# Performance work log

Measured on AMD Instinct MI355X. Metric: run time of the kernel, lower is better.

Reference implementation:

```python
import jax, jax.numpy as jnp
import numpy as np


def setup_inputs() -> dict:
    key = jax.random.key(0)
    x = jax.random.normal(key, (32, 512, 56, 56), dtype=jnp.float32)
    return {"x": x}


def reference(x):
    n, c, h, w = x.shape
    f = x.reshape(n, c, h * w)                       # (n, c, hw)
    f_norm = jax.nn.softmax(f * 7.0, axis=2)         # softmax over spatial
    bilinear = jnp.einsum('ncs,nds->ncd', f_norm, f) # (n, c, c)
    bilinear = jax.nn.softmax(bilinear, axis=2)      # softmax over channel 'keys'
    trilinear = jnp.einsum('ncd,nds->ncs', bilinear, f).reshape(n, c, h, w)
    trilinear = jax.lax.stop_gradient(trilinear)     # matches torch .detach()
    structure_att = jnp.sum(trilinear, axis=1, keepdims=True)  # (n, 1, h, w)
    return structure_att
```

## Files before the change

kernel.cpp:

```cpp
#include <hip/hip_runtime.h>
#include <stdint.h>


#define NB 32
#define CC 512
#define SS 3136
#define SCALE 7.0f
#define K7F 10.098865286222744f
#define INVK7F 0.09902102579427789f

typedef float f32x4 __attribute__((ext_vector_type(4)));
typedef _Float16 f16x8 __attribute__((ext_vector_type(8)));
typedef _Float16 f16x4 __attribute__((ext_vector_type(4)));
typedef _Float16 f16x2 __attribute__((ext_vector_type(2)));

__device__ inline unsigned short f2bf(float f) {
  unsigned int u = __float_as_uint(f);
  u += 0x7fffu + ((u >> 16) & 1u);
  return (unsigned short)(u >> 16);
}
__device__ inline float bf2f(unsigned short u) {
  return __uint_as_float((uint32_t)u << 16);
}

__device__ inline float fast_exp2(float v) {
  float r;
  asm("v_exp_f32 %0, %1" : "=v"(r) : "v"(v));
  return r;
}
__device__ inline uint32_t pk2h(float a, float b) {
  uint32_t r;
  asm("v_cvt_pkrtz_f16_f32 %0, %1, %2" : "=v"(r) : "v"(a), "v"(b));
  return r;
}
__device__ inline f16x8 exp2_f16x8(f16x8 h) {
  f16x8 r;
#pragma unroll
  for (int q = 0; q < 4; q++) {
    const float e0 = fast_exp2((float)h[2 * q]);
    const float e1 = fast_exp2((float)h[2 * q + 1]);
    ((uint32_t*)&r)[q] = pk2h(e0, e1);
  }
  return r;
}

__device__ inline float wredmax(float v) {
#pragma unroll
  for (int m = 32; m >= 1; m >>= 1) v = fmaxf(v, __shfl_xor(v, m, 64));
  return v;
}
__device__ inline float wredsum(float v) {
#pragma unroll
  for (int m = 32; m >= 1; m >>= 1) v += __shfl_xor(v, m, 64);
  return v;
}

__device__ inline void load_lds16(const void* g, void* l) {
  __builtin_amdgcn_global_load_lds(
      (const __attribute__((address_space(1))) void*)(uintptr_t)g,
      (__attribute__((address_space(3))) void*)(uintptr_t)l, 16, 0, 0);
}

__global__ __launch_bounds__(256) void k_prep(const float* __restrict__ x,
                                              unsigned short* __restrict__ t,
                                              float* __restrict__ inv7,
                                              float* __restrict__ mxv,
                                              float* __restrict__ esum) {
  const int row = blockIdx.x;
  const int tid = threadIdx.x;
  if (tid == 0) esum[row] = 0.f;
  const float4* xr = (const float4*)(x + (size_t)row * SS);
  float4 v0 = xr[tid];
  float4 v1 = xr[tid + 256];
  float4 v2 = xr[tid + 512];
  float4 v3 = (tid < 16) ? xr[768 + tid] : make_float4(-1e30f, -1e30f, -1e30f, -1e30f);

  float mx = fmaxf(fmaxf(fmaxf(v0.x, v0.y), fmaxf(v0.z, v0.w)),
             fmaxf(fmaxf(fmaxf(v1.x, v1.y), fmaxf(v1.z, v1.w)),
             fmaxf(fmaxf(fmaxf(v2.x, v2.y), fmaxf(v2.z, v2.w)),
                   fmaxf(fmaxf(v3.x, v3.y), fmaxf(v3.z, v3.w)))));
  __shared__ float redm[4], reds[4];
  mx = wredmax(mx);
  if ((tid & 63) == 0) redm[tid >> 6] = mx;
  __syncthreads();
  mx = fmaxf(fmaxf(redm[0], redm[1]), fmaxf(redm[2], redm[3]));

  float s = 0.f;
  f16x4 p0, p1, p2, p3;
#define TQ2(dst, i0, a0, a1)                                  \
  {                                                           \
    _Float16 h0 = (_Float16)(K7F * ((a0) - mx));              \
    _Float16 h1 = (_Float16)(K7F * ((a1) - mx));              \
    dst[i0] = h0; dst[i0 + 1] = h1;                           \
    uint32_t u = pk2h(fast_exp2((float)h0), fast_exp2((float)h1)); \
    f16x2 e2; *(uint32_t*)&e2 = u;                            \
    s += (float)e2[0] + (float)e2[1];                         \
  }
  TQ2(p0, 0, v0.x, v0.y) TQ2(p0, 2, v0.z, v0.w)
  TQ2(p1, 0, v1.x, v1.y) TQ2(p1, 2, v1.z, v1.w)
  TQ2(p2, 0, v2.x, v2.y) TQ2(p2, 2, v2.z, v2.w)
  TQ2(p3, 0, v3.x, v3.y) TQ2(p3, 2, v3.z, v3.w)
#undef TQ2
  s = wredsum(s);
  if ((tid & 63) == 0) reds[tid >> 6] = s;
  __syncthreads();

  f16x4* tr = (f16x4*)(t + (size_t)row * SS);
  tr[tid] = p0;
  tr[tid + 256] = p1;
  tr[tid + 512] = p2;
  if (tid < 16) tr[768 + tid] = p3;
  if (tid == 0) {
    const float stot = reds[0] + reds[1] + reds[2] + reds[3];
    inv7[row] = 1.0f / (K7F * stot);
    mxv[row] = mx;
  }
}

#define BM 128
#define BK 64
#define NT (SS / BK)

__global__ __launch_bounds__(256, 2) void k_gemm(const unsigned short* __restrict__ T,
                                                 unsigned short* __restrict__ P,
                                                 const float* __restrict__ inv7,
                                                 const float* __restrict__ mxv,
                                                 float* __restrict__ esum) {
  __shared__ unsigned short sA[2][BM * BK];
  __shared__ unsigned short sB[2][BM * BK];
  const int lin  = blockIdx.y * gridDim.x + blockIdx.x;
  const int xcd  = lin & 7;
  const int slot = lin >> 3;
  const int pair = xcd * 16 + (slot >> 2);
  const int n    = pair >> 2;
  const int tm   = (pair & 3) * BM;
  const int tn   = (slot & 3) * BM;
  const unsigned short* Ap = T + (size_t)n * CC * SS + (size_t)tm * SS;
  const unsigned short* Bp = T + (size_t)n * CC * SS + (size_t)tn * SS;
  const int tid  = threadIdx.x;
  const int lane = tid & 63;
  const int wave = tid >> 6;
  const int wm   = (wave >> 1) * 64;
  const int wn   = (wave & 1) * 64;
  const int quad = lane >> 4;
  const int rr   = lane & 15;

  int jb[4];
  const unsigned short *Aaddr[4], *Baddr[4];
#pragma unroll
  for (int tt = 0; tt < 4; tt++) {
    const int j  = ((tt << 2) + wave) * 64 + lane;
    const int r  = j >> 3;
    const int cg = (j & 7) ^ (r & 7);
    jb[tt]   = j * 8;
    Aaddr[tt] = Ap + (size_t)r * SS + cg * 8;
    Baddr[tt] = Bp + (size_t)r * SS + cg * 8;
  }

  f32x4 acc[4][4] = {};

#define COMPUTE(BUF)                                                          \
  {                                                                           \
    _Pragma("unroll")                                                         \
    for (int ki = 0; ki < 2; ki++) {                                          \
      f16x8 af[4], bfr[4];                                                    \
      const int cg = ki * 4 + quad;                                           \
      _Pragma("unroll")                                                       \
      for (int mt = 0; mt < 4; mt++) {                                        \
        const int r  = wm + mt * 16 + rr;                                     \
        const int cs = cg ^ (r & 7);                                          \
        af[mt] = *(const f16x8*)&sA[BUF][(r * 8 + cs) * 8];                   \
      }                                                                       \
      _Pragma("unroll")                                                       \
      for (int nt = 0; nt < 4; nt++) {                                        \
        const int r  = wn + nt * 16 + rr;                                     \
        const int cs = cg ^ (r & 7);                                          \
        bfr[nt] = *(const f16x8*)&sB[BUF][(r * 8 + cs) * 8];                  \
      }                                                                       \
      _Pragma("unroll")                                                       \
      for (int mt = 0; mt < 4; mt++)                                          \
        _Pragma("unroll")                                                     \
        for (int nt = 0; nt < 4; nt++)                                        \
          acc[mt][nt] = __builtin_amdgcn_mfma_f32_16x16x32_f16(               \
              af[mt], bfr[nt], acc[mt][nt], 0, 0, 0);                         \
    }                                                                         \
  }

  {
    f16x8 hv[4];
#pragma unroll
    for (int tt = 0; tt < 4; tt++) hv[tt] = *(const f16x8*)Aaddr[tt];
#pragma unroll
    for (int tt = 0; tt < 4; tt++) load_lds16(Baddr[tt], &sB[0][jb[tt]]);
#pragma unroll
    for (int tt = 0; tt < 4; tt++) *(f16x8*)&sA[0][jb[tt]] = exp2_f16x8(hv[tt]);
    __syncthreads();
  }

  int cur = 0;
  for (int t = 0; t < NT - 1; t++) {
    const int koff = (t + 1) * BK;
    const int nxt  = cur ^ 1;
    f16x8 hvN[4];
#pragma unroll
    for (int tt = 0; tt < 4; tt++) hvN[tt] = *(const f16x8*)(Aaddr[tt] + koff);
#pragma unroll
    for (int tt = 0; tt < 4; tt++) load_lds16(Baddr[tt] + koff, &sB[nxt][jb[tt]]);

    COMPUTE(cur);

#pragma unroll
    for (int tt = 0; tt < 4; tt++) *(f16x8*)&sA[nxt][jb[tt]] = exp2_f16x8(hvN[tt]);
    __syncthreads();
    cur = nxt;
  }
  COMPUTE(cur);

  unsigned short* Pp = P + ((size_t)n << 18);
  float mxd[4];
#pragma unroll
  for (int nt = 0; nt < 4; nt++) mxd[nt] = mxv[n * CC + tn + wn + nt * 16 + rr];
#pragma unroll
  for (int mt = 0; mt < 4; mt++) {
    const int rbase = tm + wm + mt * 16 + quad * 4;
    float iv[4];
#pragma unroll
    for (int i = 0; i < 4; i++) iv[i] = inv7[n * CC + rbase + i];
    float rs[4] = {0.f, 0.f, 0.f, 0.f};
#pragma unroll
    for (int nt = 0; nt < 4; nt++) {
      const int col = tn + wn + nt * 16 + rr;
#pragma unroll
      for (int i = 0; i < 4; i++) {
        const float e = __expf(acc[mt][nt][i] * iv[i] + mxd[nt]);
        rs[i] += e;
        Pp[(size_t)(rbase + i) * CC + col] = f2bf(e);
      }
    }
#pragma unroll
    for (int i = 0; i < 4; i++) {
      float v = rs[i];
#pragma unroll
      for (int m = 8; m >= 1; m >>= 1) v += __shfl_xor(v, m, 64);
      if (rr == 0) atomicAdd(&esum[n * CC + rbase + i], v);
    }
  }
#undef COMPUTE
}

__global__ __launch_bounds__(256) void k_wsum(const unsigned short* __restrict__ P,
                                              const float* __restrict__ esum,
                                              float* __restrict__ wp,
                                              float* __restrict__ outz) {
  const int lin  = blockIdx.y * gridDim.x + blockIdx.x;
  const int xcd  = lin & 7;
  const int slot = lin >> 3;
  const int n    = xcd * 4 + (slot & 3);
  const int g    = (slot >> 2) & 7;
  const int d    = (slot >> 5) * 256 + threadIdx.x;
  __shared__ float sinv[64];
  if (threadIdx.x < 64) sinv[threadIdx.x] = 1.0f / esum[n * CC + g * 64 + threadIdx.x];
  __syncthreads();
  const unsigned short* p = P + (size_t)n * CC * CC + (size_t)(g * 64) * CC + d;
  float acc = 0.f;
#pragma unroll 8
  for (int c = 0; c < 64; c++) acc += bf2f(p[(size_t)c * CC]) * sinv[c];
  wp[((size_t)n * 8 + g) * CC + d] = acc;
  const int idx = lin * 256 + threadIdx.x;
  if (idx < NB * SS) outz[idx] = 0.f;
}

__global__ __launch_bounds__(256) void k_out(const unsigned short* __restrict__ T,
                                             const float* __restrict__ wp,
                                             const float* __restrict__ mxv,
                                             float* __restrict__ out) {
  const int n  = blockIdx.y >> 2;
  const int dq = blockIdx.y & 3;
  const int s0 = (blockIdx.x * 256 + threadIdx.x) * 2;
  __shared__ float sw[128];
  __shared__ float sc[2];
  if (threadIdx.x < 128) {
    float v = 0.f;
#pragma unroll
    for (int g = 0; g < 8; g++) v += wp[((size_t)n * 8 + g) * CC + dq * 128 + threadIdx.x];
    sw[threadIdx.x] = v * INVK7F;
    float pm = v * mxv[n * CC + dq * 128 + threadIdx.x];
    pm = wredsum(pm);
    if ((threadIdx.x & 63) == 0) sc[threadIdx.x >> 6] = pm;
  }
  __syncthreads();
  const float csum = sc[0] + sc[1];
  if (s0 >= SS) return;
  const unsigned short* bp = T + (size_t)n * CC * SS + (size_t)(dq * 128) * SS + s0;
  float a0 = 0.f, a1 = 0.f;
#pragma unroll 8
  for (int d = 0; d < 128; d++) {
    const f16x2 hv = *(const f16x2*)(bp + (size_t)d * SS);
    a0 += sw[d] * (float)hv[0];
    a1 += sw[d] * (float)hv[1];
  }
  atomicAdd(&out[(size_t)n * SS + s0], a0 + csum);
  atomicAdd(&out[(size_t)n * SS + s0 + 1], a1 + csum);
}

extern "C" void kernel_launch(void* const* d_in, const int* in_sizes, int n_in,
                              void* d_out, int out_size, void* d_ws, size_t ws_size,
                              hipStream_t stream) {
  const float* x = (const float*)d_in[0];
  float* out = (float*)d_out;
  char* ws = (char*)d_ws;
  unsigned short* t    = (unsigned short*)ws;
  unsigned short* pmat = (unsigned short*)(ws + 102760448ull);
  float* esum = (float*)(ws + 119537664ull);
  float* inv7 = (float*)(ws + 119603200ull);
  float* mxv  = (float*)(ws + 119668736ull);
  float* wp   = (float*)(ws + 119734272ull);

  hipLaunchKernelGGL(k_prep, dim3(NB * CC),   dim3(256), 0, stream, x, t, inv7, mxv, esum);
  hipLaunchKernelGGL(k_gemm, dim3(16, NB),    dim3(256), 0, stream, t, pmat, inv7, mxv, esum);
  hipLaunchKernelGGL(k_wsum, dim3(16, NB),    dim3(256), 0, stream, pmat, esum, wp, out);
  hipLaunchKernelGGL(k_out,  dim3(7, NB * 4), dim3(256), 0, stream, t, wp, mxv, out);
}
```

Measured before the change: 145.9 us.

## Split GEMM K dimension in two with separate exp/softmax-sum kernel

The bilinear GEMM now splits the spatial reduction into two halves, doubling the block count, shrinking the K tile to 32 and raising occupancy to 4 blocks per CU. Each half writes fp32 partial results to a new workspace buffer. A new k_blexp kernel sums the two halves and applies the exp, bf16 store and per-row esum reduction, which replaces the atomics in the GEMM epilogue. k_out also processes 4 spatial elements per thread. The split adds about 64MB of fp32 partial traffic and one more launch, in exchange for better load balance across CUs.

```diff
diff --git a/kernel.cpp b/kernel.cpp
--- a/kernel.cpp
+++ b/kernel.cpp
@@ -64,11 +64,9 @@
 __global__ __launch_bounds__(256) void k_prep(const float* __restrict__ x,
                                               unsigned short* __restrict__ t,
                                               float* __restrict__ inv7,
-                                              float* __restrict__ mxv,
-                                              float* __restrict__ esum) {
+                                              float* __restrict__ mxv) {
   const int row = blockIdx.x;
   const int tid = threadIdx.x;
-  if (tid == 0) esum[row] = 0.f;
   const float4* xr = (const float4*)(x + (size_t)row * SS);
   float4 v0 = xr[tid];
   float4 v1 = xr[tid + 256];
@@ -118,25 +116,25 @@
 }
 
 #define BM 128
-#define BK 64
-#define NT (SS / BK)
-
-__global__ __launch_bounds__(256, 2) void k_gemm(const unsigned short* __restrict__ T,
-                                                 unsigned short* __restrict__ P,
-                                                 const float* __restrict__ inv7,
-                                                 const float* __restrict__ mxv,
-                                                 float* __restrict__ esum) {
-  __shared__ unsigned short sA[2][BM * BK];
-  __shared__ unsigned short sB[2][BM * BK];
+#define BK2 32
+#define NT2 ((SS / 2) / BK2)
+
+__global__ __launch_bounds__(256, 4) void k_gemm(const unsigned short* __restrict__ T,
+                                                 float* __restrict__ bl) {
+  __shared__ unsigned short sA[2][BM * BK2];
+  __shared__ unsigned short sB[2][BM * BK2];
   const int lin  = blockIdx.y * gridDim.x + blockIdx.x;
   const int xcd  = lin & 7;
-  const int slot = lin >> 3;
-  const int pair = xcd * 16 + (slot >> 2);
-  const int n    = pair >> 2;
-  const int tm   = (pair & 3) * BM;
-  const int tn   = (slot & 3) * BM;
-  const unsigned short* Ap = T + (size_t)n * CC * SS + (size_t)tm * SS;
-  const unsigned short* Bp = T + (size_t)n * CC * SS + (size_t)tn * SS;
+  const int idx  = lin >> 3;
+  const int n    = xcd * 4 + (idx & 3);
+  const int rest = idx >> 2;
+  const int ks   = rest & 1;
+  const int tile = rest >> 1;
+  const int tm   = (tile & 3) * BM;
+  const int tn   = (tile >> 2) * BM;
+  const int kbase = ks * (SS / 2);
+  const unsigned short* Ap = T + (size_t)n * CC * SS + (size_t)tm * SS + kbase;
+  const unsigned short* Bp = T + (size_t)n * CC * SS + (size_t)tn * SS + kbase;
   const int tid  = threadIdx.x;
   const int lane = tid & 63;
   const int wave = tid >> 6;
@@ -145,13 +143,13 @@
   const int quad = lane >> 4;
   const int rr   = lane & 15;
 
-  int jb[4];
-  const unsigned short *Aaddr[4], *Baddr[4];
-#pragma unroll
-  for (int tt = 0; tt < 4; tt++) {
-    const int j  = ((tt << 2) + wave) * 64 + lane;
-    const int r  = j >> 3;
-    const int cg = (j & 7) ^ (r & 7);
+  int jb[2];
+  const unsigned short *Aaddr[2], *Baddr[2];
+#pragma unroll
+  for (int tt = 0; tt < 2; tt++) {
+    const int j  = tt * 256 + tid;
+    const int r  = j >> 2;
+    const int cg = (j & 3) ^ (r & 3);
     jb[tt]   = j * 8;
     Aaddr[tt] = Ap + (size_t)r * SS + cg * 8;
     Baddr[tt] = Bp + (size_t)r * SS + cg * 8;
@@ -161,91 +159,107 @@
 
 #define COMPUTE(BUF)                                                          \
   {                                                                           \
+    f16x8 af[4], bfr[4];                                                      \
     _Pragma("unroll")                                                         \
-    for (int ki = 0; ki < 2; ki++) {                                          \
-      f16x8 af[4], bfr[4];                                                    \
-      const int cg = ki * 4 + quad;                                           \
+    for (int mt = 0; mt < 4; mt++) {                                          \
+      const int r  = wm + mt * 16 + rr;                                       \
+      const int cs = quad ^ (r & 3);                                          \
+      af[mt] = *(const f16x8*)&sA[BUF][(r * 4 + cs) * 8];                     \
+    }                                                                         \
+    _Pragma("unroll")                                                         \
+    for (int nt = 0; nt < 4; nt++) {                                          \
+      const int r  = wn + nt * 16 + rr;                                       \
+      const int cs = quad ^ (r & 3);                                          \
+      bfr[nt] = *(const f16x8*)&sB[BUF][(r * 4 + cs) * 8];                    \
+    }                                                                         \
+    _Pragma("unroll")                                                         \
+    for (int mt = 0; mt < 4; mt++)                                            \
       _Pragma("unroll")                                                       \
-      for (int mt = 0; mt < 4; mt++) {                                        \
-        const int r  = wm + mt * 16 + rr;                                     \
-        const int cs = cg ^ (r & 7);                                          \
-        af[mt] = *(const f16x8*)&sA[BUF][(r * 8 + cs) * 8];                   \
-      }                                                                       \
-      _Pragma("unroll")                                                       \
-      for (int nt = 0; nt < 4; nt++) {                                        \
-        const int r  = wn + nt * 16 + rr;                                     \
-        const int cs = cg ^ (r & 7);                                          \
-        bfr[nt] = *(const f16x8*)&sB[BUF][(r * 8 + cs) * 8];                  \
-      }                                                                       \
-      _Pragma("unroll")                                                       \
-      for (int mt = 0; mt < 4; mt++)                                          \
-        _Pragma("unroll")                                                     \
-        for (int nt = 0; nt < 4; nt++)                                        \
-          acc[mt][nt] = __builtin_amdgcn_mfma_f32_16x16x32_f16(               \
-              af[mt], bfr[nt], acc[mt][nt], 0, 0, 0);                         \
-    }                                                                         \
+      for (int nt = 0; nt < 4; nt++)                                          \
+        acc[mt][nt] = __builtin_amdgcn_mfma_f32_16x16x32_f16(                 \
+            af[mt], bfr[nt], acc[mt][nt], 0, 0, 0);                           \
   }
 
   {
-    f16x8 hv[4];
-#pragma unroll
-    for (int tt = 0; tt < 4; tt++) hv[tt] = *(const f16x8*)Aaddr[tt];
-#pragma unroll
-    for (int tt = 0; tt < 4; tt++) load_lds16(Baddr[tt], &sB[0][jb[tt]]);
-#pragma unroll
-    for (int tt = 0; tt < 4; tt++) *(f16x8*)&sA[0][jb[tt]] = exp2_f16x8(hv[tt]);
+    f16x8 hv[2];
+#pragma unroll
+    for (int tt = 0; tt < 2; tt++) load_lds16(Baddr[tt], &sB[0][jb[tt]]);
+#pragma unroll
+    for (int tt = 0; tt < 2; tt++) hv[tt] = *(const f16x8*)Aaddr[tt];
+#pragma unroll
+    for (int tt = 0; tt < 2; tt++) *(f16x8*)&sA[0][jb[tt]] = exp2_f16x8(hv[tt]);
     __syncthreads();
   }
 
   int cur = 0;
-  for (int t = 0; t < NT - 1; t++) {
-    const int koff = (t + 1) * BK;
-    const int nxt  = cur ^ 1;
-    f16x8 hvN[4];
-#pragma unroll
-    for (int tt = 0; tt < 4; tt++) hvN[tt] = *(const f16x8*)(Aaddr[tt] + koff);
-#pragma unroll
-    for (int tt = 0; tt < 4; tt++) load_lds16(Baddr[tt] + koff, &sB[nxt][jb[tt]]);
+  for (int t = 0; t < NT2 - 1; t++) {
+    const int ko  = (t + 1) * BK2;
+    const int nxt = cur ^ 1;
+    f16x8 hvN[2];
+#pragma unroll
+    for (int tt = 0; tt < 2; tt++) load_lds16(Baddr[tt] + ko, &sB[nxt][jb[tt]]);
+#pragma unroll
+    for (int tt = 0; tt < 2; tt++) hvN[tt] = *(const f16x8*)(Aaddr[tt] + ko);
 
     COMPUTE(cur);
 
 #pragma unroll
-    for (int tt = 0; tt < 4; tt++) *(f16x8*)&sA[nxt][jb[tt]] = exp2_f16x8(hvN[tt]);
+    for (int tt = 0; tt < 2; tt++) *(f16x8*)&sA[nxt][jb[tt]] = exp2_f16x8(hvN[tt]);
     __syncthreads();
     cur = nxt;
   }
   COMPUTE(cur);
 
-  unsigned short* Pp = P + ((size_t)n << 18);
-  float mxd[4];
-#pragma unroll
-  for (int nt = 0; nt < 4; nt++) mxd[nt] = mxv[n * CC + tn + wn + nt * 16 + rr];
+  float* Bl = bl + (size_t)ks * 8388608ull + (size_t)n * CC * CC;
 #pragma unroll
   for (int mt = 0; mt < 4; mt++) {
     const int rbase = tm + wm + mt * 16 + quad * 4;
-    float iv[4];
-#pragma unroll
-    for (int i = 0; i < 4; i++) iv[i] = inv7[n * CC + rbase + i];
-    float rs[4] = {0.f, 0.f, 0.f, 0.f};
 #pragma unroll
     for (int nt = 0; nt < 4; nt++) {
       const int col = tn + wn + nt * 16 + rr;
 #pragma unroll
-      for (int i = 0; i < 4; i++) {
-        const float e = __expf(acc[mt][nt][i] * iv[i] + mxd[nt]);
-        rs[i] += e;
-        Pp[(size_t)(rbase + i) * CC + col] = f2bf(e);
-      }
+      for (int i = 0; i < 4; i++)
+        Bl[(size_t)(rbase + i) * CC + col] = acc[mt][nt][i];
     }
-#pragma unroll
-    for (int i = 0; i < 4; i++) {
-      float v = rs[i];
-#pragma unroll
-      for (int m = 8; m >= 1; m >>= 1) v += __shfl_xor(v, m, 64);
-      if (rr == 0) atomicAdd(&esum[n * CC + rbase + i], v);
-    }
   }
 #undef COMPUTE
+}
+
+__global__ __launch_bounds__(256) void k_blexp(const float* __restrict__ bl,
+                                               const float* __restrict__ inv7,
+                                               const float* __restrict__ mxv,
+                                               unsigned short* __restrict__ P,
+                                               float* __restrict__ esum) {
+  const int lin = blockIdx.y * gridDim.x + blockIdx.x;
+  const int xcd = lin & 7;
+  const int idx = lin >> 3;
+  const int n   = xcd * 4 + (idx & 3);
+  const int r0  = (idx >> 2) * 8;
+  const int tid = threadIdx.x;
+  const int c0  = tid * 2;
+  const float mx0 = mxv[n * CC + c0];
+  const float mx1 = mxv[n * CC + c0 + 1];
+  __shared__ float red[4];
+  const float* b0 = bl + (size_t)n * CC * CC;
+  const float* b1 = b0 + 8388608ull;
+  unsigned short* Pp = P + ((size_t)n << 18);
+#pragma unroll 2
+  for (int r = 0; r < 8; r++) {
+    const int row = r0 + r;
+    const float iv = inv7[n * CC + row];
+    const float2 v0 = *(const float2*)&b0[(size_t)row * CC + c0];
+    const float2 v1 = *(const float2*)&b1[(size_t)row * CC + c0];
+    const float e0 = __expf(iv * (v0.x + v1.x) + mx0);
+    const float e1 = __expf(iv * (v0.y + v1.y) + mx1);
+    *(uint32_t*)&Pp[(size_t)row * CC + c0] =
+        ((uint32_t)f2bf(e1) << 16) | (uint32_t)f2bf(e0);
+    float s = e0 + e1;
+    s = wredsum(s);
+    if ((tid & 63) == 0) red[tid >> 6] = s;
+    __syncthreads();
+    if (tid == 0) esum[n * CC + row] = red[0] + red[1] + red[2] + red[3];
+    __syncthreads();
+  }
 }
 
 __global__ __launch_bounds__(256) void k_wsum(const unsigned short* __restrict__ P,
@@ -276,7 +290,7 @@
                                              float* __restrict__ out) {
   const int n  = blockIdx.y >> 2;
   const int dq = blockIdx.y & 3;
-  const int s0 = (blockIdx.x * 256 + threadIdx.x) * 2;
+  const int s0 = (blockIdx.x * 256 + threadIdx.x) * 4;
   __shared__ float sw[128];
   __shared__ float sc[2];
   if (threadIdx.x < 128) {
@@ -292,15 +306,19 @@
   const float csum = sc[0] + sc[1];
   if (s0 >= SS) return;
   const unsigned short* bp = T + (size_t)n * CC * SS + (size_t)(dq * 128) * SS + s0;
-  float a0 = 0.f, a1 = 0.f;
+  float a0 = 0.f, a1 = 0.f, a2 = 0.f, a3 = 0.f;
 #pragma unroll 8
   for (int d = 0; d < 128; d++) {
-    const f16x2 hv = *(const f16x2*)(bp + (size_t)d * SS);
+    const f16x4 hv = *(const f16x4*)(bp + (size_t)d * SS);
     a0 += sw[d] * (float)hv[0];
     a1 += sw[d] * (float)hv[1];
-  }
-  atomicAdd(&out[(size_t)n * SS + s0], a0 + csum);
+    a2 += sw[d] * (float)hv[2];
+    a3 += sw[d] * (float)hv[3];
+  }
+  atomicAdd(&out[(size_t)n * SS + s0],     a0 + csum);
   atomicAdd(&out[(size_t)n * SS + s0 + 1], a1 + csum);
+  atomicAdd(&out[(size_t)n * SS + s0 + 2], a2 + csum);
+  atomicAdd(&out[(size_t)n * SS + s0 + 3], a3 + csum);
 }
 
 extern "C" void kernel_launch(void* const* d_in, const int* in_sizes, int n_in,
@@ -311,13 +329,15 @@
   char* ws = (char*)d_ws;
   unsigned short* t    = (unsigned short*)ws;
   unsigned short* pmat = (unsigned short*)(ws + 102760448ull);
-  float* esum = (float*)(ws + 119537664ull);
-  float* inv7 = (float*)(ws + 119603200ull);
-  float* mxv  = (float*)(ws + 119668736ull);
-  float* wp   = (float*)(ws + 119734272ull);
-
-  hipLaunchKernelGGL(k_prep, dim3(NB * CC),   dim3(256), 0, stream, x, t, inv7, mxv, esum);
-  hipLaunchKernelGGL(k_gemm, dim3(16, NB),    dim3(256), 0, stream, t, pmat, inv7, mxv, esum);
-  hipLaunchKernelGGL(k_wsum, dim3(16, NB),    dim3(256), 0, stream, pmat, esum, wp, out);
-  hipLaunchKernelGGL(k_out,  dim3(7, NB * 4), dim3(256), 0, stream, t, wp, mxv, out);
-}
+  float* bl   = (float*)(ws + 119537664ull);
+  float* esum = (float*)(ws + 186646528ull);
+  float* inv7 = (float*)(ws + 186712064ull);
+  float* mxv  = (float*)(ws + 186777600ull);
+  float* wp   = (float*)(ws + 186843136ull);
+
+  hipLaunchKernelGGL(k_prep,  dim3(NB * CC),   dim3(256), 0, stream, x, t, inv7, mxv);
+  hipLaunchKernelGGL(k_gemm,  dim3(32, NB),    dim3(256), 0, stream, t, bl);
+  hipLaunchKernelGGL(k_blexp, dim3(64, NB),    dim3(256), 0, stream, bl, inv7, mxv, pmat, esum);
+  hipLaunchKernelGGL(k_wsum,  dim3(16, NB),    dim3(256), 0, stream, pmat, esum, wp, out);
+  hipLaunchKernelGGL(k_out,   dim3(4, NB * 4), dim3(256), 0, stream, t, wp, mxv, out);
+}
```

Result: slower. 164.0 us (+12.4%).
